# Performance work log

Hardware: AMD Instinct MI355X
Metric: run time of the kernel (lower is better)

The kernel has to match this reference:

```python
import jax, jax.numpy as jnp
import numpy as np

B, S, D = 4, 2048, 2048
NH, NKV = 16, 4
HD = D // NH  # 128


def setup_inputs() -> dict:
    key = jax.random.key(0)
    ks = jax.random.split(key, 6)
    sd = 1.0 / np.sqrt(D)
    return {
        "x": jax.random.normal(ks[0], (B, S, D), jnp.float32),
        "cos": jax.random.normal(ks[1], (1, 1, S, HD), jnp.float32),
        "sin": jax.random.normal(ks[2], (1, 1, S, HD), jnp.float32),
        "wq_w": jax.random.normal(ks[3], (D, D), jnp.float32) * sd,
        "wk_w": jax.random.normal(ks[4], (NKV * HD, D), jnp.float32) * sd,
        "wv_w": jax.random.normal(ks[5], (NKV * HD, D), jnp.float32) * sd,
        "start_pos": 0,
    }


def _rotate_half(t):
    h = t.shape[-1] // 2
    return jnp.concatenate([-t[..., h:], t[..., :h]], axis=-1)


def reference(x, cos, sin, wq_w, wk_w, wv_w, start_pos):
    b, s, d = x.shape
    n_rep = NH // NKV
    q = (x @ wq_w.T).reshape(b, s, NH, HD).transpose(0, 2, 1, 3)      # [b,H,s,hd]
    k = (x @ wk_w.T).reshape(b, s, NKV, HD).transpose(0, 2, 1, 3)     # [b,Hk,s,hd]
    v = (x @ wv_w.T).reshape(b, s, NKV, HD).transpose(0, 2, 1, 3)
    # rotary
    q = q * cos + _rotate_half(q) * sin
    k = k * cos + _rotate_half(k) * sin
    # repeat_kv
    k = jnp.repeat(k, n_rep, axis=1)   # [b,H,s,hd]
    v = jnp.repeat(v, n_rep, axis=1)
    scores = jnp.einsum("bhqd,bhkd->bhqk", q, k) / jnp.sqrt(jnp.float32(HD))
    causal = jnp.tril(jnp.ones((s, s), dtype=bool))
    scores = jnp.where(causal, scores, jnp.float32(-jnp.inf))
    w = jax.nn.softmax(scores, axis=-1)
    out = jnp.einsum("bhqk,bhkd->bhqd", w, v)
    return out.transpose(0, 2, 1, 3).reshape(b, s, d)
```

## Files before the change

kernel.cpp:

```cpp
#include <hip/hip_runtime.h>
#include <hip/hip_bf16.h>
#include <math.h>

#define B_ 4
#define S_ 2048
#define D_ 2048
#define NH_ 16
#define NKV_ 4
#define HD_ 128

typedef short bf16x8 __attribute__((ext_vector_type(8)));
typedef float f32x4 __attribute__((ext_vector_type(4)));
typedef __hip_bfloat16 bf16;

#define ASYNC_CP16(gp, lp)                                                    \
  __builtin_amdgcn_global_load_lds(                                           \
      (const __attribute__((address_space(1))) unsigned int*)(gp),            \
      (__attribute__((address_space(3))) unsigned int*)(lp), 16, 0, 0)

__device__ __forceinline__ short f2b(float f) {
  union { bf16 h; short s; } u;
  u.h = __float2bfloat16(f);
  return u.s;
}

__global__ __launch_bounds__(256) void cvt_kernel(const float* __restrict__ in,
                                                  bf16* __restrict__ out, int n4) {
  int i = blockIdx.x * 256 + threadIdx.x;
  if (i >= n4) return;
  float4 v = ((const float4*)in)[i];
  union { ushort4 u; bf16 h[4]; } o;
  o.h[0] = __float2bfloat16(v.x);
  o.h[1] = __float2bfloat16(v.y);
  o.h[2] = __float2bfloat16(v.z);
  o.h[3] = __float2bfloat16(v.w);
  ((ushort4*)out)[i] = o.u;
}

__global__ __launch_bounds__(256) void gemm_bt(const bf16* __restrict__ A,
                                               const bf16* __restrict__ Bm,
                                               bf16* __restrict__ C,
                                               int M, int N, int K) {
  __shared__ __align__(16) bf16 As[128 * 64];
  __shared__ __align__(16) bf16 Bs[128 * 64];
  const int tid = threadIdx.x;
  const int lane = tid & 63, wave = tid >> 6;
  const int wm = (wave & 1) * 64, wn = (wave >> 1) * 64;
  const int m0 = blockIdx.x * 128, n0 = blockIdx.y * 128;
  const int quad = lane >> 4, c = lane & 15;

  f32x4 acc[4][4] = {};

  const int sr = lane >> 3;
  const int sg = lane & 7;
  const int gc = (sg ^ sr) * 8;
  const bf16* Ap = A + (size_t)(m0 + wave * 32 + sr) * K + gc;
  const bf16* Bp = Bm + (size_t)(n0 + wave * 32 + sr) * K + gc;

  for (int kb = 0; kb < K; kb += 64) {
    __syncthreads();
#pragma unroll
    for (int i = 0; i < 4; i++) {
      ASYNC_CP16(Ap + (size_t)(i * 8) * K + kb, &As[(wave * 32 + i * 8) * 64]);
      ASYNC_CP16(Bp + (size_t)(i * 8) * K + kb, &Bs[(wave * 32 + i * 8) * 64]);
    }
    __syncthreads();
#pragma unroll
    for (int kk = 0; kk < 2; kk++) {
      const int slot = ((kk * 4 + quad) ^ (c & 7)) * 8;
      bf16x8 af[4], bfr[4];
#pragma unroll
      for (int t = 0; t < 4; t++) {
        af[t]  = *(const bf16x8*)(&As[(wm + t * 16 + c) * 64 + slot]);
        bfr[t] = *(const bf16x8*)(&Bs[(wn + t * 16 + c) * 64 + slot]);
      }
#pragma unroll
      for (int mt = 0; mt < 4; mt++)
#pragma unroll
        for (int nt = 0; nt < 4; nt++)
          acc[mt][nt] = __builtin_amdgcn_mfma_f32_16x16x32_bf16(
              af[mt], bfr[nt], acc[mt][nt], 0, 0, 0);
    }
  }
#pragma unroll
  for (int mt = 0; mt < 4; mt++)
#pragma unroll
    for (int nt = 0; nt < 4; nt++)
#pragma unroll
      for (int reg = 0; reg < 4; reg++) {
        int row = m0 + wm + mt * 16 + quad * 4 + reg;
        int col = n0 + wn + nt * 16 + c;
        C[(size_t)row * N + col] = __float2bfloat16(acc[mt][nt][reg]);
      }
}

__global__ __launch_bounds__(256) void rope_relayout(
    const bf16* __restrict__ in, int instride, const float* __restrict__ cosp,
    const float* __restrict__ sinp, bf16* __restrict__ out, int nh, float scale) {
  int idx = blockIdx.x * 256 + threadIdx.x;
  int d = idx & 63;
  int t = idx >> 6;
  int h = t % nh; t /= nh;
  int s = t % S_;
  int b = t / S_;
  const bf16* p = in + (size_t)(b * S_ + s) * instride + h * HD_;
  float q1 = __bfloat162float(p[d]);
  float q2 = __bfloat162float(p[d + 64]);
  float c1 = cosp[s * HD_ + d], c2 = cosp[s * HD_ + d + 64];
  float s1 = sinp[s * HD_ + d], s2 = sinp[s * HD_ + d + 64];
  float o1 = (q1 * c1 - q2 * s1) * scale;
  float o2 = (q2 * c2 + q1 * s2) * scale;
  bf16* q = out + ((size_t)(b * nh + h) * S_ + s) * HD_;
  q[d] = __float2bfloat16(o1);
  q[d + 64] = __float2bfloat16(o2);
}

__global__ __launch_bounds__(256) void v_transpose(const bf16* __restrict__ in,
                                                   int instride,
                                                   bf16* __restrict__ out) {
  __shared__ __align__(16) bf16 tile[64][HD_ + 8];
  int bidx = blockIdx.x;
  int st = bidx & 31;
  int kv = (bidx >> 5) & 3;
  int b = bidx >> 7;
  int s0 = st * 64;
  int t = threadIdx.x;
  {
    int row = t >> 2;
    int colb = (t & 3) * 32;
#pragma unroll
    for (int i = 0; i < 4; i++) {
      int col = colb + i * 8;
      *(uint4*)(&tile[row][col]) = *(const uint4*)(
          &in[(size_t)(b * S_ + s0 + row) * instride + kv * HD_ + col]);
    }
  }
  __syncthreads();
  int sl = t & 63, hb = t >> 6;
#pragma unroll
  for (int i = 0; i < 32; i++) {
    int hd = i * 4 + hb;
    out[((size_t)(b * NKV_ + kv) * HD_ + hd) * S_ + s0 + sl] = tile[sl][hd];
  }
}

__device__ __forceinline__ void attn_step(
    const bf16* __restrict__ Ks, const bf16* __restrict__ Vs,
    bf16* __restrict__ Psw, const bf16x8* qf, f32x4* o,
    float& m_i, float& l_i, bool diag, int kb, int qbase, int quad, int c) {
  f32x4 sacc[4] = {};
#pragma unroll
  for (int kt = 0; kt < 4; kt++) {
    const int slot = ((kt * 4 + quad) ^ (c & 7)) * 8;
#pragma unroll
    for (int mt = 0; mt < 4; mt++) {
      bf16x8 kf = *(const bf16x8*)(&Ks[(mt * 16 + c) * 128 + slot]);
      sacc[mt] = __builtin_amdgcn_mfma_f32_16x16x32_bf16(kf, qf[kt], sacc[mt], 0, 0, 0);
    }
  }
  if (diag) {
    const int qg = qbase + c;
#pragma unroll
    for (int mt = 0; mt < 4; mt++)
#pragma unroll
      for (int r = 0; r < 4; r++)
        if (kb + mt * 16 + quad * 4 + r > qg) sacc[mt][r] = -INFINITY;
  }
  float mx = sacc[0][0];
#pragma unroll
  for (int mt = 0; mt < 4; mt++)
#pragma unroll
    for (int r = 0; r < 4; r++) mx = fmaxf(mx, sacc[mt][r]);
  mx = fmaxf(mx, __shfl_xor(mx, 16, 64));
  mx = fmaxf(mx, __shfl_xor(mx, 32, 64));
  const float mnew = fmaxf(m_i, mx);
  const float alpha = exp2f(m_i - mnew);
  m_i = mnew;
  float rs = 0.f;
#pragma unroll
  for (int mt = 0; mt < 4; mt++) {
    short4 pk;
    float p0 = exp2f(sacc[mt][0] - mnew);
    float p1 = exp2f(sacc[mt][1] - mnew);
    float p2 = exp2f(sacc[mt][2] - mnew);
    float p3 = exp2f(sacc[mt][3] - mnew);
    rs += (p0 + p1) + (p2 + p3);
    pk.x = f2b(p0); pk.y = f2b(p1); pk.z = f2b(p2); pk.w = f2b(p3);
    *(short4*)(&Psw[c * 72 + mt * 16 + quad * 4]) = pk;
  }
  rs += __shfl_xor(rs, 16, 64);
  rs += __shfl_xor(rs, 32, 64);
  l_i = l_i * alpha + rs;
  if (__any(alpha != 1.0f)) {
    float a0 = __shfl(alpha, quad * 4 + 0, 64);
    float a1 = __shfl(alpha, quad * 4 + 1, 64);
    float a2 = __shfl(alpha, quad * 4 + 2, 64);
    float a3 = __shfl(alpha, quad * 4 + 3, 64);
#pragma unroll
    for (int nt = 0; nt < 8; nt++) {
      o[nt][0] *= a0; o[nt][1] *= a1; o[nt][2] *= a2; o[nt][3] *= a3;
    }
  }
#pragma unroll
  for (int kk = 0; kk < 2; kk++) {
    bf16x8 pf = *(const bf16x8*)(&Psw[c * 72 + kk * 32 + quad * 8]);
    const int slot = ((kk * 4 + quad) ^ (c & 7)) * 8;
#pragma unroll
    for (int nt = 0; nt < 8; nt++) {
      bf16x8 vf = *(const bf16x8*)(&Vs[(nt * 16 + c) * 64 + slot]);
      o[nt] = __builtin_amdgcn_mfma_f32_16x16x32_bf16(pf, vf, o[nt], 0, 0, 0);
    }
  }
}

__global__ __launch_bounds__(256) void attn_kernel(const bf16* __restrict__ Q,
                                                   const bf16* __restrict__ Kr,
                                                   const bf16* __restrict__ Vt,
                                                   float* __restrict__ O) {
  __shared__ __align__(16) bf16 Ks[64 * 128];
  __shared__ __align__(16) bf16 Vs[128 * 64];
  __shared__ __align__(16) bf16 Ps[4][16 * 72];

  const int tid = threadIdx.x, lane = tid & 63, wave = tid >> 6;
  const int quad = lane >> 4, c = lane & 15;
  const int j = blockIdx.x;
  const int bh = blockIdx.y;
  const int b = bh >> 4, h = bh & 15, kv = h >> 2;
  bf16* Psw = &Ps[wave][0];

  const bf16* kbase = Kr + (size_t)(b * NKV_ + kv) * S_ * HD_;
  const bf16* vbase = Vt + (size_t)(b * NKV_ + kv) * HD_ * S_;

  int koff[4], voff;
  {
    const int kl = lane >> 4;
    const int ks = lane & 15;
#pragma unroll
    for (int i = 0; i < 4; i++) {
      int r = wave * 16 + i * 4 + kl;
      koff[i] = r * HD_ + ((ks ^ (r & 7)) * 8);
    }
    const int vl = lane >> 3;
    const int vs = lane & 7;
    voff = (wave * 32 + vl) * S_ + ((vs ^ (vl & 7)) * 8);
  }

#pragma unroll 1
  for (int pass = 0; pass < 2; ++pass) {
    const int qt = pass ? (31 - j) : j;
    const int q0 = qt * 64;
    const int qb = q0 + wave * 16;

    bf16x8 qf[4];
    {
      const bf16* qp = Q + ((size_t)(b * NH_ + h) * S_ + qb + c) * HD_;
#pragma unroll
      for (int kt = 0; kt < 4; kt++)
        qf[kt] = *(const bf16x8*)(qp + kt * 32 + quad * 8);
    }
    f32x4 o_acc[8] = {};
    float m_i = -INFINITY, l_i = 0.f;

#pragma unroll 1
    for (int it = 0; it <= qt; ++it) {
      const int kb = it * 64;
      __syncthreads();
#pragma unroll
      for (int i = 0; i < 4; i++) {
        ASYNC_CP16(kbase + (size_t)kb * HD_ + koff[i], &Ks[(wave * 16 + i * 4) * 128]);
        ASYNC_CP16(vbase + kb + voff + (size_t)(i * 8) * S_, &Vs[(wave * 32 + i * 8) * 64]);
      }
      __syncthreads();
      attn_step(Ks, Vs, Psw, qf, o_acc, m_i, l_i, it == qt, kb, qb, quad, c);
    }

    float inv[4];
#pragma unroll
    for (int r = 0; r < 4; r++) inv[r] = 1.0f / __shfl(l_i, quad * 4 + r, 64);
    float* obase = O + (size_t)b * S_ * D_ + (size_t)h * HD_;
#pragma unroll
    for (int nt = 0; nt < 8; nt++)
#pragma unroll
      for (int r = 0; r < 4; r++)
        obase[(size_t)(qb + quad * 4 + r) * D_ + nt * 16 + c] = o_acc[nt][r] * inv[r];
  }
}

extern "C" void kernel_launch(void* const* d_in, const int* in_sizes, int n_in,
                              void* d_out, int out_size, void* d_ws, size_t ws_size,
                              hipStream_t stream) {
  const float* x    = (const float*)d_in[0];
  const float* cosp = (const float*)d_in[1];
  const float* sinp = (const float*)d_in[2];
  const float* wq   = (const float*)d_in[3];
  const float* wk   = (const float*)d_in[4];
  const float* wv   = (const float*)d_in[5];
  float* out = (float*)d_out;

  char* ws = (char*)d_ws;
  const size_t MB = 1024 * 1024;
  bf16* xb    = (bf16*)(ws + 0);
  bf16* qr    = (bf16*)(ws + 0);
  bf16* wqkvb = (bf16*)(ws + 32 * MB);
  bf16* qkv   = (bf16*)(ws + 44 * MB);
  bf16* kr    = (bf16*)(ws + 92 * MB);
  bf16* vt    = (bf16*)(ws + 100 * MB);

  cvt_kernel<<<16384, 256, 0, stream>>>(x, xb, 4194304);
  cvt_kernel<<<4096, 256, 0, stream>>>(wq, wqkvb, 1048576);
  cvt_kernel<<<1024, 256, 0, stream>>>(wk, wqkvb + 4194304, 262144);
  cvt_kernel<<<1024, 256, 0, stream>>>(wv, wqkvb + 5242880, 262144);

  gemm_bt<<<dim3(64, 24), 256, 0, stream>>>(xb, wqkvb, qkv, 8192, 3072, 2048);

  const float qscale = 1.4426950408889634f / 11.313708498984761f;
  rope_relayout<<<32768, 256, 0, stream>>>(qkv, 3072, cosp, sinp, qr, NH_, qscale);
  rope_relayout<<<8192, 256, 0, stream>>>(qkv + 2048, 3072, cosp, sinp, kr, NKV_, 1.0f);
  v_transpose<<<512, 256, 0, stream>>>(qkv + 2560, 3072, vt);

  attn_kernel<<<dim3(16, 64), 256, 0, stream>>>(qr, kr, vt, out);
}
```

Baseline: 434.3 us.

## Fuse RoPE and head relayout into QKV GEMM epilogue; faster bf16 pack

The QKV projection GEMM now has each block cover one full 128-wide head. Each wave owns 32 rows across all 128 columns, so the rotary pairs d and d+64 sit in the same thread. RoPE, the softmax scale and the per-head relayout are applied in the epilogue, which removes the separate rope_relayout launches and the round trip of the intermediate qkv buffer. V is written densely for the existing transpose kernel. In attention, the P-to-bf16 pack switches to an add-and-perm rounding trick. That trick skips NaN handling and uses round-half-up instead of round-to-nearest-even, and the new wave tiling reuses fewer A fragments per B load.

```diff
diff --git a/kernel.cpp b/kernel.cpp
--- a/kernel.cpp
+++ b/kernel.cpp
@@ -17,12 +17,6 @@
   __builtin_amdgcn_global_load_lds(                                           \
       (const __attribute__((address_space(1))) unsigned int*)(gp),            \
       (__attribute__((address_space(3))) unsigned int*)(lp), 16, 0, 0)
-
-__device__ __forceinline__ short f2b(float f) {
-  union { bf16 h; short s; } u;
-  u.h = __float2bfloat16(f);
-  return u.s;
-}
 
 __global__ __launch_bounds__(256) void cvt_kernel(const float* __restrict__ in,
                                                   bf16* __restrict__ out, int n4) {
@@ -37,25 +31,28 @@
   ((ushort4*)out)[i] = o.u;
 }
 
-__global__ __launch_bounds__(256) void gemm_bt(const bf16* __restrict__ A,
-                                               const bf16* __restrict__ Bm,
-                                               bf16* __restrict__ C,
-                                               int M, int N, int K) {
+__global__ __launch_bounds__(256) void gemm_qkv(
+    const bf16* __restrict__ A, const bf16* __restrict__ W,
+    bf16* __restrict__ qr, bf16* __restrict__ kr, bf16* __restrict__ vlin,
+    const float* __restrict__ cosp, const float* __restrict__ sinp,
+    float qscale) {
   __shared__ __align__(16) bf16 As[128 * 64];
   __shared__ __align__(16) bf16 Bs[128 * 64];
   const int tid = threadIdx.x;
   const int lane = tid & 63, wave = tid >> 6;
-  const int wm = (wave & 1) * 64, wn = (wave >> 1) * 64;
-  const int m0 = blockIdx.x * 128, n0 = blockIdx.y * 128;
+  const int m0 = blockIdx.x * 128;
+  const int hblk = blockIdx.y;
+  const int n0 = hblk * 128;
   const int quad = lane >> 4, c = lane & 15;
-
-  f32x4 acc[4][4] = {};
+  const int K = 2048;
+
+  f32x4 acc[2][8] = {};
 
   const int sr = lane >> 3;
   const int sg = lane & 7;
   const int gc = (sg ^ sr) * 8;
   const bf16* Ap = A + (size_t)(m0 + wave * 32 + sr) * K + gc;
-  const bf16* Bp = Bm + (size_t)(n0 + wave * 32 + sr) * K + gc;
+  const bf16* Bp = W + (size_t)(n0 + wave * 32 + sr) * K + gc;
 
   for (int kb = 0; kb < K; kb += 64) {
     __syncthreads();
@@ -68,51 +65,58 @@
 #pragma unroll
     for (int kk = 0; kk < 2; kk++) {
       const int slot = ((kk * 4 + quad) ^ (c & 7)) * 8;
-      bf16x8 af[4], bfr[4];
-#pragma unroll
-      for (int t = 0; t < 4; t++) {
-        af[t]  = *(const bf16x8*)(&As[(wm + t * 16 + c) * 64 + slot]);
-        bfr[t] = *(const bf16x8*)(&Bs[(wn + t * 16 + c) * 64 + slot]);
-      }
-#pragma unroll
-      for (int mt = 0; mt < 4; mt++)
-#pragma unroll
-        for (int nt = 0; nt < 4; nt++)
+      bf16x8 af[2], bfr[8];
+#pragma unroll
+      for (int t = 0; t < 2; t++)
+        af[t] = *(const bf16x8*)(&As[(wave * 32 + t * 16 + c) * 64 + slot]);
+#pragma unroll
+      for (int t = 0; t < 8; t++)
+        bfr[t] = *(const bf16x8*)(&Bs[(t * 16 + c) * 64 + slot]);
+#pragma unroll
+      for (int mt = 0; mt < 2; mt++)
+#pragma unroll
+        for (int nt = 0; nt < 8; nt++)
           acc[mt][nt] = __builtin_amdgcn_mfma_f32_16x16x32_bf16(
               af[mt], bfr[nt], acc[mt][nt], 0, 0, 0);
     }
   }
-#pragma unroll
-  for (int mt = 0; mt < 4; mt++)
-#pragma unroll
-    for (int nt = 0; nt < 4; nt++)
+
+  if (hblk < 20) {
+    const float scale = (hblk < 16) ? qscale : 1.0f;
+#pragma unroll
+    for (int mt = 0; mt < 2; mt++)
 #pragma unroll
       for (int reg = 0; reg < 4; reg++) {
-        int row = m0 + wm + mt * 16 + quad * 4 + reg;
-        int col = n0 + wn + nt * 16 + c;
-        C[(size_t)row * N + col] = __float2bfloat16(acc[mt][nt][reg]);
+        int m = m0 + wave * 32 + mt * 16 + quad * 4 + reg;
+        int b = m >> 11, s = m & 2047;
+        const float* cr = cosp + s * HD_;
+        const float* sn = sinp + s * HD_;
+        bf16* orow = (hblk < 16)
+            ? qr + ((size_t)(b * NH_ + hblk) * S_ + s) * HD_
+            : kr + ((size_t)(b * NKV_ + (hblk - 16)) * S_ + s) * HD_;
+#pragma unroll
+        for (int nt = 0; nt < 4; nt++) {
+          int d1 = nt * 16 + c, d2 = d1 + 64;
+          float q1 = acc[mt][nt][reg], q2 = acc[mt][nt + 4][reg];
+          float o1 = (q1 * cr[d1] - q2 * sn[d1]) * scale;
+          float o2 = (q2 * cr[d2] + q1 * sn[d2]) * scale;
+          orow[d1] = __float2bfloat16(o1);
+          orow[d2] = __float2bfloat16(o2);
+        }
       }
-}
-
-__global__ __launch_bounds__(256) void rope_relayout(
-    const bf16* __restrict__ in, int instride, const float* __restrict__ cosp,
-    const float* __restrict__ sinp, bf16* __restrict__ out, int nh, float scale) {
-  int idx = blockIdx.x * 256 + threadIdx.x;
-  int d = idx & 63;
-  int t = idx >> 6;
-  int h = t % nh; t /= nh;
-  int s = t % S_;
-  int b = t / S_;
-  const bf16* p = in + (size_t)(b * S_ + s) * instride + h * HD_;
-  float q1 = __bfloat162float(p[d]);
-  float q2 = __bfloat162float(p[d + 64]);
-  float c1 = cosp[s * HD_ + d], c2 = cosp[s * HD_ + d + 64];
-  float s1 = sinp[s * HD_ + d], s2 = sinp[s * HD_ + d + 64];
-  float o1 = (q1 * c1 - q2 * s1) * scale;
-  float o2 = (q2 * c2 + q1 * s2) * scale;
-  bf16* q = out + ((size_t)(b * nh + h) * S_ + s) * HD_;
-  q[d] = __float2bfloat16(o1);
-  q[d + 64] = __float2bfloat16(o2);
+  } else {
+    bf16* vbase = vlin + (size_t)(hblk - 20) * HD_;
+#pragma unroll
+    for (int mt = 0; mt < 2; mt++)
+#pragma unroll
+      for (int reg = 0; reg < 4; reg++) {
+        int m = m0 + wave * 32 + mt * 16 + quad * 4 + reg;
+        bf16* row = vbase + (size_t)m * (NKV_ * HD_);
+#pragma unroll
+        for (int nt = 0; nt < 8; nt++)
+          row[nt * 16 + c] = __float2bfloat16(acc[mt][nt][reg]);
+      }
+  }
 }
 
 __global__ __launch_bounds__(256) void v_transpose(const bf16* __restrict__ in,
@@ -179,14 +183,19 @@
   float rs = 0.f;
 #pragma unroll
   for (int mt = 0; mt < 4; mt++) {
-    short4 pk;
     float p0 = exp2f(sacc[mt][0] - mnew);
     float p1 = exp2f(sacc[mt][1] - mnew);
     float p2 = exp2f(sacc[mt][2] - mnew);
     float p3 = exp2f(sacc[mt][3] - mnew);
     rs += (p0 + p1) + (p2 + p3);
-    pk.x = f2b(p0); pk.y = f2b(p1); pk.z = f2b(p2); pk.w = f2b(p3);
-    *(short4*)(&Psw[c * 72 + mt * 16 + quad * 4]) = pk;
+    unsigned u0 = __builtin_bit_cast(unsigned, p0) + 0x8000u;
+    unsigned u1 = __builtin_bit_cast(unsigned, p1) + 0x8000u;
+    unsigned u2 = __builtin_bit_cast(unsigned, p2) + 0x8000u;
+    unsigned u3 = __builtin_bit_cast(unsigned, p3) + 0x8000u;
+    uint2 pk;
+    pk.x = __builtin_amdgcn_perm(u1, u0, 0x07060302u);
+    pk.y = __builtin_amdgcn_perm(u3, u2, 0x07060302u);
+    *(uint2*)(&Psw[c * 72 + mt * 16 + quad * 4]) = pk;
   }
   rs += __shfl_xor(rs, 16, 64);
   rs += __shfl_xor(rs, 32, 64);
@@ -300,23 +309,22 @@
   char* ws = (char*)d_ws;
   const size_t MB = 1024 * 1024;
   bf16* xb    = (bf16*)(ws + 0);
-  bf16* qr    = (bf16*)(ws + 0);
   bf16* wqkvb = (bf16*)(ws + 32 * MB);
-  bf16* qkv   = (bf16*)(ws + 44 * MB);
-  bf16* kr    = (bf16*)(ws + 92 * MB);
-  bf16* vt    = (bf16*)(ws + 100 * MB);
+  bf16* qr    = (bf16*)(ws + 44 * MB);
+  bf16* kr    = (bf16*)(ws + 76 * MB);
+  bf16* vlin  = (bf16*)(ws + 84 * MB);
+  bf16* vt    = (bf16*)(ws + 92 * MB);
 
   cvt_kernel<<<16384, 256, 0, stream>>>(x, xb, 4194304);
   cvt_kernel<<<4096, 256, 0, stream>>>(wq, wqkvb, 1048576);
   cvt_kernel<<<1024, 256, 0, stream>>>(wk, wqkvb + 4194304, 262144);
   cvt_kernel<<<1024, 256, 0, stream>>>(wv, wqkvb + 5242880, 262144);
 
-  gemm_bt<<<dim3(64, 24), 256, 0, stream>>>(xb, wqkvb, qkv, 8192, 3072, 2048);
-
   const float qscale = 1.4426950408889634f / 11.313708498984761f;
-  rope_relayout<<<32768, 256, 0, stream>>>(qkv, 3072, cosp, sinp, qr, NH_, qscale);
-  rope_relayout<<<8192, 256, 0, stream>>>(qkv + 2048, 3072, cosp, sinp, kr, NKV_, 1.0f);
-  v_transpose<<<512, 256, 0, stream>>>(qkv + 2560, 3072, vt);
+  gemm_qkv<<<dim3(64, 24), 256, 0, stream>>>(xb, wqkvb, qr, kr, vlin,
+                                             cosp, sinp, qscale);
+
+  v_transpose<<<512, 256, 0, stream>>>(vlin, NKV_ * HD_, vt);
 
   attn_kernel<<<dim3(16, 64), 256, 0, stream>>>(qr, kr, vt, out);
 }
```

Result: no change. 426.2 us (-1.9%).
